# Kernel tuning notes

Measured on AMD Instinct MI355X. Metric: run time of the kernel, lower is better.

Reference implementation:

```python
import jax, jax.numpy as jnp
import numpy as np

N = 50000      # nodes per graph
E = 800000     # edges per graph (avg degree 16)
IN = 128       # in_dim
OUT = 64       # out_dim
HEADS = 2      # second GCNConv out = OUT*HEADS = 128
FILL = 2.0     # improved=True self-loop weight


def setup_inputs():
    key = jax.random.key(0)
    ks = jax.random.split(key, 10)
    x1 = jax.random.normal(ks[0], (N, IN), jnp.float32)
    edge_index1 = jax.random.randint(ks[1], (2, E), 0, N)
    edge_weight1 = jax.random.uniform(ks[2], (E,), jnp.float32)
    x2 = jax.random.normal(ks[3], (N, IN), jnp.float32)
    edge_index2 = jax.random.randint(ks[4], (2, E), 0, N)
    edge_weight2 = jax.random.uniform(ks[5], (E,), jnp.float32)
    # shared tower params (source bug: gcn1 used for both inputs)
    W1 = jax.random.normal(ks[6], (IN, OUT), jnp.float32) / np.sqrt(IN)
    b1 = jnp.zeros((OUT,), jnp.float32)
    W2 = jax.random.normal(ks[7], (OUT, OUT * HEADS), jnp.float32) / np.sqrt(OUT)
    b2 = jnp.zeros((OUT * HEADS,), jnp.float32)
    return {"x1": x1, "edge_index1": edge_index1, "edge_weight1": edge_weight1,
            "x2": x2, "edge_index2": edge_index2, "edge_weight2": edge_weight2,
            "W1": W1, "b1": b1, "W2": W2, "b2": b2}


def _gcn_conv(x, src, dst, ew, W, b, n):
    # GCNConv(improved=True, add_self_loops=True, aggr='max')
    loop = jnp.arange(n)
    src = jnp.concatenate([src, loop])
    dst = jnp.concatenate([dst, loop])
    ew = jnp.concatenate([ew, jnp.full((n,), FILL, ew.dtype)])
    # symmetric gcn normalization
    deg = jax.ops.segment_sum(ew, dst, num_segments=n)
    dinv = jnp.where(deg > 0, jax.lax.rsqrt(jnp.maximum(deg, 1e-30)), 0.0)
    norm = dinv[src] * ew * dinv[dst]          # [E+N]
    h = x @ W                                   # [N, F_out]
    msg = norm[:, None] * h[src]                # [E+N, F_out] gathered messages
    out = jax.ops.segment_max(msg, dst, num_segments=n)  # scatter-max
    out = jnp.where(jnp.isfinite(out), out, 0.0)          # guard empty segments
    return out + b


def _tower(x, ei, ew, W1, b1, W2, b2):
    ew = jax.nn.relu(ew)
    h = _gcn_conv(x, ei[0], ei[1], ew, W1, b1, x.shape[0])
    return _gcn_conv(h, ei[0], ei[1], ew, W2, b2, x.shape[0])


def reference(x1, edge_index1, edge_weight1, x2, edge_index2, edge_weight2, W1, b1, W2, b2):
    g1 = _tower(x1, edge_index1, edge_weight1, W1, b1, W2, b2)
    g2 = _tower(x2, edge_index2, edge_weight2, W1, b1, W2, b2)
    return (g1, g2)
```

## Files before the change

### kernel.cpp

```cpp
#include <hip/hip_runtime.h>
#include <hip/hip_fp16.h>

static constexpr float FILLW = 2.0f;
static constexpr int BSH  = 6;
static constexpr int CAPB = 1792;
static constexpr int NPB  = 256;
static constexpr int EPT  = 8;

__device__ __forceinline__ unsigned pk_mul(unsigned a, unsigned b){
    unsigned r; asm("v_pk_mul_f16 %0, %1, %2" : "=v"(r) : "v"(a), "v"(b)); return r;
}
__device__ __forceinline__ unsigned pk_max(unsigned a, unsigned b){
    unsigned r; asm("v_pk_max_f16 %0, %1, %2" : "=v"(r) : "v"(a), "v"(b)); return r;
}

template<int F, int K, int TR, int KC, bool SCALE, typename OutT>
__device__ __forceinline__ void gemm_tile(const float* __restrict__ A,
        const float* __restrict__ W, OutT* __restrict__ C,
        const float* __restrict__ dv, int rb, int N,
        float* __restrict__ Ws, float* __restrict__ As){
    constexpr int NCH = K / KC;
    constexpr int TRp = TR;
    constexpr int CG  = F / 8;
    constexpr int LPT = TR * KC / 1024;
    const int tid = threadIdx.x;
    for (int i = tid; i < K * F / 4; i += 256)
        ((float4*)Ws)[i] = ((const float4*)W)[i];
    const int tx = tid % CG, ty = tid / CG;
    const int c0 = tx * 8, r0 = ty * 8;

    float acc[8][8];
    #pragma unroll
    for (int i = 0; i < 8; ++i)
        #pragma unroll
        for (int j = 0; j < 8; ++j) acc[i][j] = 0.f;

    float4 st[LPT];
    auto gload = [&](int kc){
        #pragma unroll
        for (int l2 = 0; l2 < LPT; ++l2){
            int l = l2 * 256 + tid;
            int r = l / (KC / 4);
            int kk = (l % (KC / 4)) * 4;
            int ar = rb + r; if (ar >= N) ar = N - 1;
            st[l2] = *(const float4*)(A + (size_t)ar * K + kc * KC + kk);
        }
    };
    auto swrite = [&](int buf){
        float* p = As + buf * (KC * TRp);
        #pragma unroll
        for (int l2 = 0; l2 < LPT; ++l2){
            int l = l2 * 256 + tid;
            int r = l / (KC / 4);
            int kk = (l % (KC / 4)) * 4;
            p[(kk+0)*TRp + r] = st[l2].x;
            p[(kk+1)*TRp + r] = st[l2].y;
            p[(kk+2)*TRp + r] = st[l2].z;
            p[(kk+3)*TRp + r] = st[l2].w;
        }
    };

    gload(0); swrite(0);
    __syncthreads();
    for (int kc = 0; kc < NCH; ++kc){
        if (kc + 1 < NCH) gload(kc + 1);
        const float* Ab = As + (kc & 1) * (KC * TRp);
        #pragma unroll
        for (int j = 0; j < KC; ++j){
            const float* wrow = Ws + (kc * KC + j) * F + c0;
            float4 w0 = *(const float4*)(wrow);
            float4 w1 = *(const float4*)(wrow + 4);
            float4 a0 = *(const float4*)(Ab + j * TRp + r0);
            float4 a1 = *(const float4*)(Ab + j * TRp + r0 + 4);
            float av[8] = {a0.x,a0.y,a0.z,a0.w,a1.x,a1.y,a1.z,a1.w};
            float wvv[8] = {w0.x,w0.y,w0.z,w0.w,w1.x,w1.y,w1.z,w1.w};
            #pragma unroll
            for (int rr = 0; rr < 8; ++rr)
                #pragma unroll
                for (int cc = 0; cc < 8; ++cc)
                    acc[rr][cc] = fmaf(av[rr], wvv[cc], acc[rr][cc]);
        }
        if (kc + 1 < NCH){ swrite((kc + 1) & 1); __syncthreads(); }
    }
    #pragma unroll
    for (int rr = 0; rr < 8; ++rr){
        int row = rb + r0 + rr;
        if (row < N){
            float scv = 1.0f;
            if constexpr (SCALE) scv = dv[row];
            if constexpr (sizeof(OutT) == 2){
                __half2 o2[4];
                #pragma unroll
                for (int q = 0; q < 4; ++q)
                    o2[q] = __floats2half2_rn(acc[rr][2*q]*scv, acc[rr][2*q+1]*scv);
                *(float4*)((__half*)C + (size_t)row * F + c0) = *(float4*)o2;
            } else {
                float4 o0 = {acc[rr][0]*scv, acc[rr][1]*scv, acc[rr][2]*scv, acc[rr][3]*scv};
                float4 o1 = {acc[rr][4]*scv, acc[rr][5]*scv, acc[rr][6]*scv, acc[rr][7]*scv};
                *(float4*)((float*)C + (size_t)row * F + c0)     = o0;
                *(float4*)((float*)C + (size_t)row * F + c0 + 4) = o1;
            }
        }
    }
}

__device__ __forceinline__ void xcd_map(int c, int TW2, int LIN_BPT,
                                        int& t, int& chunk){
    if (TW2){ int x = c & 7; t = x >> 2; chunk = (c >> 3) * 4 + (x & 3); }
    else    { t = c / LIN_BPT; chunk = c - t * LIN_BPT; }
}

__global__ void __launch_bounds__(256) k_cg1(const float* __restrict__ x0,
        const float* __restrict__ x1, const float* __restrict__ W1,
        __half* __restrict__ h0, __half* __restrict__ h1,
        const int* __restrict__ dst0, const int* __restrict__ dst1,
        int* __restrict__ cnts,
        int N, int E, int BPT, int GB, int B1, int TW2){
    __shared__ float Ws[64 * 128];
    __shared__ float As[2 * 8 * 256];
    if ((int)blockIdx.x < GB){
        int t  = (int)blockIdx.x / BPT;
        int rb = ((int)blockIdx.x - t * BPT) * 256;
        gemm_tile<64,128,256,8,false,__half>(t ? x1 : x0, W1, t ? h1 : h0,
                                             nullptr, rb, N, Ws, As);
        return;
    }
    int t, blk;
    xcd_map((int)blockIdx.x - GB, TW2, NPB, t, blk);
    const int* dst = t ? dst1 : dst0;
    int* hist = (int*)Ws;
    const int tid = threadIdx.x;
    for (int i = tid; i < B1; i += 256) hist[i] = 0;
    __syncthreads();
    int per = (E + NPB - 1) / NPB;
    int e0 = blk * per;
    int e1 = e0 + per; if (e1 > E) e1 = E;
    for (int e = e0 + tid; e < e1; e += 256 * EPT){
        int dl[EPT];
        #pragma unroll
        for (int q = 0; q < EPT; ++q){ int ee = e + q*256; dl[q] = (ee < e1) ? dst[ee] : -1; }
        #pragma unroll
        for (int q = 0; q < EPT; ++q) if (dl[q] >= 0) atomicAdd(&hist[dl[q] >> BSH], 1);
    }
    __syncthreads();
    int* co = cnts + (size_t)(t * NPB + blk) * B1;
    for (int i = tid; i < B1; i += 256) co[i] = hist[i];
}

__global__ void __launch_bounds__(64) k_scanR(int* __restrict__ cnts,
        int* __restrict__ gcnt, int B1){
    int bid = (int)blockIdx.x;
    int t = bid / B1, b = bid % B1;
    int lane = threadIdx.x;
    int* cp = cnts + (size_t)t * NPB * B1 + b;
    int x[4];
    #pragma unroll
    for (int j = 0; j < 4; ++j) x[j] = cp[(size_t)(lane * 4 + j) * B1];
    int s = x[0] + x[1] + x[2] + x[3];
    int sc = s;
    #pragma unroll
    for (int o = 1; o < 64; o <<= 1){ int u = __shfl_up(sc, o); if (lane >= o) sc += u; }
    int e0 = sc - s;
    int e1 = e0 + x[0], e2 = e1 + x[1], e3 = e2 + x[2];
    cp[(size_t)(lane * 4 + 0) * B1] = e0;
    cp[(size_t)(lane * 4 + 1) * B1] = e1;
    cp[(size_t)(lane * 4 + 2) * B1] = e2;
    cp[(size_t)(lane * 4 + 3) * B1] = e3;
    if (lane == 63) gcnt[t * B1 + b] = sc;
}

__global__ void __launch_bounds__(256) k_scatter(const int* __restrict__ src0,
        const int* __restrict__ src1,
        const int* __restrict__ dst0, const int* __restrict__ dst1,
        const float* __restrict__ ew0, const float* __restrict__ ew1,
        const int* __restrict__ cnts, uint2* __restrict__ stage,
        int N, int E, int B1, int TW2){
    __shared__ int hist[1024];
    int t, blk;
    xcd_map((int)blockIdx.x, TW2, NPB, t, blk);
    const int* src = t ? src1 : src0;
    const int* dst = t ? dst1 : dst0;
    const float* ew = t ? ew1 : ew0;
    uint2* stg = stage + (size_t)t * B1 * CAPB;
    const int* co = cnts + (size_t)(t * NPB + blk) * B1;
    const int tid = threadIdx.x;
    for (int i = tid; i < B1; i += 256) hist[i] = co[i];
    __syncthreads();
    int per = (E + NPB - 1) / NPB;
    int e0 = blk * per;
    int e1 = e0 + per; if (e1 > E) e1 = E;
    for (int e = e0 + tid; e < e1; e += 256 * EPT){
        int dl[EPT], sl[EPT]; float wl[EPT];
        #pragma unroll
        for (int q = 0; q < EPT; ++q){
            int ee = e + q*256;
            if (ee < e1){ dl[q] = dst[ee]; sl[q] = src[ee]; wl[q] = fmaxf(ew[ee], 0.f); }
            else dl[q] = -1;
        }
        int r[EPT];
        #pragma unroll
        for (int q = 0; q < EPT; ++q)
            if (dl[q] >= 0) r[q] = atomicAdd(&hist[dl[q] >> BSH], 1);
        #pragma unroll
        for (int q = 0; q < EPT; ++q)
            if (dl[q] >= 0 && r[q] < CAPB)
                stg[(size_t)(dl[q] >> BSH) * CAPB + r[q]] =
                    make_uint2(__float_as_uint(wl[q]),
                               (unsigned)sl[q] | ((unsigned)(dl[q] & 63) << 16));
    }
}

__global__ void __launch_bounds__(256) k_pack(const uint2* __restrict__ stage,
        const int* __restrict__ gcnt, int* __restrict__ woff,
        uint2* __restrict__ sn, float* __restrict__ dinv,
        __half* __restrict__ h1, int N, int E, int B1, int TW2){
    int t, b;
    xcd_map((int)blockIdx.x, TW2, B1, t, b);
    if (b >= B1) return;
    const int tid = threadIdx.x;
    const uint2* stg = stage + (size_t)t * B1 * CAPB;
    const int* gc = gcnt + t * B1;
    __shared__ int   wsum[4];
    __shared__ int   nh[64];
    __shared__ float nw[64];
    __shared__ int   offs[64];
    __shared__ float dvs[64];
    int acc = 0;
    for (int i = tid; i < b; i += 256) acc += gc[i];
    #pragma unroll
    for (int o = 32; o; o >>= 1) acc += __shfl_down(acc, o);
    int lane = tid & 63, wv = tid >> 6;
    if (lane == 0) wsum[wv] = acc;
    if (tid < 64){ nh[tid] = 0; nw[tid] = 0.f; }
    __syncthreads();
    const int base = wsum[0] + wsum[1] + wsum[2] + wsum[3];
    int cnt = gc[b]; if (cnt > CAPB) cnt = CAPB;

    int   rr[7]; uint2 rec[7];
    #pragma unroll
    for (int q = 0; q < 7; ++q){
        int j = q * 256 + tid;
        if (j < cnt){
            uint2 v = stg[(size_t)b * CAPB + j];
            int nl = (v.y >> 16) & 63;
            rr[q] = atomicAdd(&nh[nl], 1);
            atomicAdd(&nw[nl], __uint_as_float(v.x));
            rec[q] = v;
        } else rec[q].y = 0xFFFFFFFFu;
    }
    __syncthreads();
    if (tid < 64){
        int v = nh[tid], sc = v;
        #pragma unroll
        for (int o = 1; o < 64; o <<= 1){ int u = __shfl_up(sc, o); if (tid >= o) sc += u; }
        offs[tid] = sc - v;
        int n = (b << BSH) + tid;
        float dv = 0.f;
        if (n < N){
            dv = rsqrtf(FILLW + nw[tid]);
            woff[t * N + n] = base + sc - v;
            dinv[t * N + n] = dv;
        }
        dvs[tid] = dv;
    }
    __syncthreads();
    uint2* sno = sn + (size_t)t * E;
    #pragma unroll
    for (int q = 0; q < 7; ++q){
        if (rec[q].y != 0xFFFFFFFFu){
            int nl   = (int)((rec[q].y >> 16) & 63);
            unsigned srcv = rec[q].y & 0xFFFFu;
            __half hw = __float2half(__uint_as_float(rec[q].x));
            unsigned hu = (unsigned)__half_as_ushort(hw);
            sno[(size_t)base + offs[nl] + rr[q]] =
                make_uint2(srcv, hu | (hu << 16));
        }
    }
    __half2* hb = (__half2*)(h1 + ((size_t)t * N + ((size_t)b << BSH)) * 64);
    #pragma unroll
    for (int j = 0; j < 8; ++j){
        int idx = j * 256 + tid;
        int r = idx >> 5, cc = idx & 31;
        if ((b << BSH) + r < N){
            float2 f = __half22float2(hb[r * 32 + cc]);
            float dv = dvs[r];
            hb[r * 32 + cc] = __floats2half2_rn(f.x * dv, f.y * dv);
        }
    }
}

__global__ void __launch_bounds__(256) k_gemm2(const float* __restrict__ A0,
        const float* __restrict__ A1, const float* __restrict__ W,
        __half* __restrict__ C0, __half* __restrict__ C1,
        const float* __restrict__ dinv, int N, int BPT){
    __shared__ float Ws[64 * 128];
    __shared__ float As[2 * 8 * 128];
    int t  = (int)blockIdx.x / BPT;
    int rb = ((int)blockIdx.x - t * BPT) * 128;
    gemm_tile<128,64,128,8,true,__half>(t ? A1 : A0, W, t ? C1 : C0,
                                        dinv + t * N, rb, N, Ws, As);
}

template<int F, int UG>
__global__ void __launch_bounds__(256) k_agg(const int* __restrict__ woff,
        const uint2* __restrict__ sn, const float* __restrict__ dinv,
        const __half* __restrict__ H0, const __half* __restrict__ H1,
        const float* __restrict__ bias, float* __restrict__ O0, float* __restrict__ O1,
        int N, int E, int BPT, int TW2){
    constexpr int LPR = F / 8;
    constexpr int EG  = 64 / LPR;
    const int lane = threadIdx.x & 63, wv = threadIdx.x >> 6;
    int t, chunk;
    xcd_map((int)blockIdx.x, TW2, BPT, t, chunk);
    int n = chunk * 4 + wv;
    if (n >= N) return;
    int g = t * N + n;
    int beg = woff[g];
    int end = (n == N - 1) ? E : woff[g + 1];
    float di = dinv[g];
    int cnt = end - beg;
    const uint2* st = sn + (size_t)t * E;
    const __half* H = t ? H1 : H0;
    float* O = t ? O1 : O0;
    const int fl = lane % LPR;
    const int eg = lane / LPR;

    unsigned acc[4];
    {
        float4 hv = *(const float4*)(H + (size_t)n * F + fl * 8);
        const unsigned* hp = (const unsigned*)&hv;
        const unsigned two2 = 0x40004000u;
        #pragma unroll
        for (int k = 0; k < 4; ++k) acc[k] = pk_mul(hp[k], two2);
    }
    for (int base = 0; base < cnt; base += 64){
        int m = cnt - base; if (m > 64) m = 64;
        uint2 er = make_uint2(0u, 0u);
        if (lane < m) er = st[beg + base + lane];
        int es = (int)er.x;
        int ep = (int)er.y;
        for (int j = 0; j < m; j += EG * UG){
            int sl[UG], wl[UG]; float4 hv[UG];
            #pragma unroll
            for (int u = 0; u < UG; ++u){
                int jj = j + u * EG + eg; if (jj > m - 1) jj = m - 1;
                sl[u] = __shfl(es, jj);
                wl[u] = __shfl(ep, jj);
            }
            #pragma unroll
            for (int u = 0; u < UG; ++u)
                hv[u] = *(const float4*)(H + (size_t)sl[u] * F + fl * 8);
            #pragma unroll
            for (int u = 0; u < UG; ++u){
                const unsigned* hp = (const unsigned*)&hv[u];
                unsigned w2 = (unsigned)wl[u];
                #pragma unroll
                for (int k = 0; k < 4; ++k)
                    acc[k] = pk_max(acc[k], pk_mul(hp[k], w2));
            }
        }
    }
    #pragma unroll
    for (int msk = LPR; msk < 64; msk <<= 1)
        #pragma unroll
        for (int k = 0; k < 4; ++k){
            unsigned o = (unsigned)__shfl_xor((int)acc[k], msk);
            acc[k] = pk_max(acc[k], o);
        }
    if constexpr (F == 128){
        int f0 = fl * 8 + eg * 2;
        float2 f = __half22float2(*(__half2*)&acc[eg]);
        float2 bb = *(const float2*)(bias + f0);
        *(float2*)(O + (size_t)n * F + f0) =
            make_float2(di * f.x + bb.x, di * f.y + bb.y);
    } else {
        int f0 = fl * 8 + eg;
        unsigned av = acc[eg >> 1];
        unsigned short hs = (unsigned short)((eg & 1) ? (av >> 16) : (av & 0xFFFFu));
        float v = __half2float(__ushort_as_half(hs));
        O[(size_t)n * F + f0] = di * v + bias[f0];
    }
}


extern "C" void kernel_launch(void* const* d_in, const int* in_sizes, int n_in,
                              void* d_out, int out_size, void* d_ws, size_t ws_size,
                              hipStream_t stream){
    const int E  = in_sizes[2];
    const int F1 = in_sizes[7];
    const int F2 = in_sizes[9];
    const int IN = in_sizes[6] / F1;
    const int N  = in_sizes[0] / IN;
    const int B1 = (N + 63) >> BSH;

    const float* W1 = (const float*)d_in[6];
    const float* b1 = (const float*)d_in[7];
    const float* W2 = (const float*)d_in[8];
    const float* b2 = (const float*)d_in[9];

    auto need = [&](int G){
        return (size_t)G * E * 8
             + (size_t)G * N * F2 * 2
             + (size_t)G * N * F1 * 4
             + (size_t)G * N * 8
             + (size_t)G * B1 * 4
             + (size_t)G * NPB * B1 * 4
             + 4096;
    };
    const int G = (ws_size >= need(2)) ? 2 : 1;
    const int TW2 = (G == 2);

    uint2*  sn    = (uint2*)d_ws;
    __half* hbuf  = (__half*)(sn + (size_t)G * E);
    float*  out1  = (float*)(hbuf + (size_t)G * N * F2);
    uint2*  stage = (uint2*)out1;
    float*  dinv  = out1 + (size_t)G * N * F1;
    int*    woff  = (int*)(dinv + (size_t)G * N);
    int*    gcnt  = woff + (size_t)G * N;
    int*    cnts  = gcnt + (size_t)G * B1;

    const int BPT1 = (N + 255) / 256;
    const int BPT2 = (N + 127) / 128;
    const int ABT  = (N + 3) / 4;
    const int GB   = G * BPT1;
    const int partGrid = TW2 ? (NPB / 4) * 8          : G * NPB;
    const int packGrid = TW2 ? ((B1 + 3) / 4) * 8     : G * B1;
    const int aggGrid  = TW2 ? ((ABT + 3) / 4) * 8    : G * ABT;

    for (int it = 0; it < 2; it += G){
        int t0 = it, t1 = (G == 2) ? it + 1 : it;
        const float* x0 = (const float*)d_in[t0*3], * x1 = (const float*)d_in[t1*3];
        const int* ei0 = (const int*)d_in[t0*3+1], * ei1 = (const int*)d_in[t1*3+1];
        const float* ew0 = (const float*)d_in[t0*3+2], * ew1 = (const float*)d_in[t1*3+2];
        const int* src0 = ei0, * dst0 = ei0 + E;
        const int* src1 = ei1, * dst1 = ei1 + E;
        __half* h1_0 = hbuf, * h1_1 = hbuf + (size_t)(G-1) * N * F1;
        __half* h2_0 = hbuf, * h2_1 = hbuf + (size_t)(G-1) * N * F2;
        float* o1_0 = out1, * o1_1 = out1 + (size_t)(G-1) * N * F1;
        float* go0 = (float*)d_out + (size_t)t0 * N * F2;
        float* go1 = (float*)d_out + (size_t)t1 * N * F2;

        k_cg1<<<GB + partGrid, 256, 0, stream>>>(x0, x1, W1, h1_0, h1_1,
                                                 dst0, dst1, cnts, N, E, BPT1, GB, B1, TW2);
        k_scanR<<<G * B1, 64, 0, stream>>>(cnts, gcnt, B1);
        k_scatter<<<partGrid, 256, 0, stream>>>(src0, src1, dst0, dst1, ew0, ew1,
                                                cnts, stage, N, E, B1, TW2);
        k_pack<<<packGrid, 256, 0, stream>>>(stage, gcnt, woff, sn, dinv, hbuf,
                                             N, E, B1, TW2);
        k_agg<64,4><<<aggGrid, 256, 0, stream>>>(woff, sn, dinv, h1_0, h1_1, b1,
                                                 o1_0, o1_1, N, E, ABT, TW2);
        k_gemm2<<<G * BPT2, 256, 0, stream>>>(o1_0, o1_1, W2, h2_0, h2_1, dinv, N, BPT2);
        k_agg<128,4><<<aggGrid, 256, 0, stream>>>(woff, sn, dinv, h2_0, h2_1, b2,
                                                  go0, go1, N, E, ABT, TW2);
    }
}
```

Baseline: 318.5 us.

## Fuse histogram, scan and scatter via global atomic bucket offsets

Replaces the per-block count write, the separate scan kernel and the separate scatter kernel with in-kernel reservation of bucket ranges through atomicAdd on global bucket counters. This is followed directly by scattering edges into staging within the same kernel. It removes two kernel launches and the per-block count matrix traffic, at the cost of global atomic contention (mitigated by rotating bucket order per block) and nondeterministic edge order within buckets. A memset zeroes the counters each iteration. The first aggregation's second template parameter is also reduced from 4 to 2.

```diff
diff --git a/kernel.cpp b/kernel.cpp
--- a/kernel.cpp
+++ b/kernel.cpp
@@ -113,8 +113,10 @@
 __global__ void __launch_bounds__(256) k_cg1(const float* __restrict__ x0,
         const float* __restrict__ x1, const float* __restrict__ W1,
         __half* __restrict__ h0, __half* __restrict__ h1,
+        const int* __restrict__ src0, const int* __restrict__ src1,
         const int* __restrict__ dst0, const int* __restrict__ dst1,
-        int* __restrict__ cnts,
+        const float* __restrict__ ew0, const float* __restrict__ ew1,
+        uint2* __restrict__ stage, int* __restrict__ gcnt,
         int N, int E, int BPT, int GB, int B1, int TW2){
     __shared__ float Ws[64 * 128];
     __shared__ float As[2 * 8 * 256];
@@ -127,7 +129,11 @@
     }
     int t, blk;
     xcd_map((int)blockIdx.x - GB, TW2, NPB, t, blk);
+    const int* src = t ? src1 : src0;
     const int* dst = t ? dst1 : dst0;
+    const float* ew = t ? ew1 : ew0;
+    uint2* stg = stage + (size_t)t * B1 * CAPB;
+    int* gc = gcnt + t * B1;
     int* hist = (int*)Ws;
     const int tid = threadIdx.x;
     for (int i = tid; i < B1; i += 256) hist[i] = 0;
@@ -143,52 +149,13 @@
         for (int q = 0; q < EPT; ++q) if (dl[q] >= 0) atomicAdd(&hist[dl[q] >> BSH], 1);
     }
     __syncthreads();
-    int* co = cnts + (size_t)(t * NPB + blk) * B1;
-    for (int i = tid; i < B1; i += 256) co[i] = hist[i];
-}
-
-__global__ void __launch_bounds__(64) k_scanR(int* __restrict__ cnts,
-        int* __restrict__ gcnt, int B1){
-    int bid = (int)blockIdx.x;
-    int t = bid / B1, b = bid % B1;
-    int lane = threadIdx.x;
-    int* cp = cnts + (size_t)t * NPB * B1 + b;
-    int x[4];
-    #pragma unroll
-    for (int j = 0; j < 4; ++j) x[j] = cp[(size_t)(lane * 4 + j) * B1];
-    int s = x[0] + x[1] + x[2] + x[3];
-    int sc = s;
-    #pragma unroll
-    for (int o = 1; o < 64; o <<= 1){ int u = __shfl_up(sc, o); if (lane >= o) sc += u; }
-    int e0 = sc - s;
-    int e1 = e0 + x[0], e2 = e1 + x[1], e3 = e2 + x[2];
-    cp[(size_t)(lane * 4 + 0) * B1] = e0;
-    cp[(size_t)(lane * 4 + 1) * B1] = e1;
-    cp[(size_t)(lane * 4 + 2) * B1] = e2;
-    cp[(size_t)(lane * 4 + 3) * B1] = e3;
-    if (lane == 63) gcnt[t * B1 + b] = sc;
-}
-
-__global__ void __launch_bounds__(256) k_scatter(const int* __restrict__ src0,
-        const int* __restrict__ src1,
-        const int* __restrict__ dst0, const int* __restrict__ dst1,
-        const float* __restrict__ ew0, const float* __restrict__ ew1,
-        const int* __restrict__ cnts, uint2* __restrict__ stage,
-        int N, int E, int B1, int TW2){
-    __shared__ int hist[1024];
-    int t, blk;
-    xcd_map((int)blockIdx.x, TW2, NPB, t, blk);
-    const int* src = t ? src1 : src0;
-    const int* dst = t ? dst1 : dst0;
-    const float* ew = t ? ew1 : ew0;
-    uint2* stg = stage + (size_t)t * B1 * CAPB;
-    const int* co = cnts + (size_t)(t * NPB + blk) * B1;
-    const int tid = threadIdx.x;
-    for (int i = tid; i < B1; i += 256) hist[i] = co[i];
-    __syncthreads();
-    int per = (E + NPB - 1) / NPB;
-    int e0 = blk * per;
-    int e1 = e0 + per; if (e1 > E) e1 = E;
+    int rot = (blk * 193) % B1;
+    for (int i = tid; i < B1; i += 256){
+        int b = i + rot; if (b >= B1) b -= B1;
+        int h = hist[b];
+        hist[b] = h ? atomicAdd(&gc[b], h) : 0;
+    }
+    __syncthreads();
     for (int e = e0 + tid; e < e1; e += 256 * EPT){
         int dl[EPT], sl[EPT]; float wl[EPT];
         #pragma unroll
@@ -404,7 +371,6 @@
              + (size_t)G * N * F1 * 4
              + (size_t)G * N * 8
              + (size_t)G * B1 * 4
-             + (size_t)G * NPB * B1 * 4
              + 4096;
     };
     const int G = (ws_size >= need(2)) ? 2 : 1;
@@ -417,7 +383,6 @@
     float*  dinv  = out1 + (size_t)G * N * F1;
     int*    woff  = (int*)(dinv + (size_t)G * N);
     int*    gcnt  = woff + (size_t)G * N;
-    int*    cnts  = gcnt + (size_t)G * B1;
 
     const int BPT1 = (N + 255) / 256;
     const int BPT2 = (N + 127) / 128;
@@ -440,14 +405,13 @@
         float* go0 = (float*)d_out + (size_t)t0 * N * F2;
         float* go1 = (float*)d_out + (size_t)t1 * N * F2;
 
+        hipMemsetAsync(gcnt, 0, (size_t)G * B1 * sizeof(int), stream);
         k_cg1<<<GB + partGrid, 256, 0, stream>>>(x0, x1, W1, h1_0, h1_1,
-                                                 dst0, dst1, cnts, N, E, BPT1, GB, B1, TW2);
-        k_scanR<<<G * B1, 64, 0, stream>>>(cnts, gcnt, B1);
-        k_scatter<<<partGrid, 256, 0, stream>>>(src0, src1, dst0, dst1, ew0, ew1,
-                                                cnts, stage, N, E, B1, TW2);
+                                                 src0, src1, dst0, dst1, ew0, ew1,
+                                                 stage, gcnt, N, E, BPT1, GB, B1, TW2);
         k_pack<<<packGrid, 256, 0, stream>>>(stage, gcnt, woff, sn, dinv, hbuf,
                                              N, E, B1, TW2);
-        k_agg<64,4><<<aggGrid, 256, 0, stream>>>(woff, sn, dinv, h1_0, h1_1, b1,
+        k_agg<64,2><<<aggGrid, 256, 0, stream>>>(woff, sn, dinv, h1_0, h1_1, b1,
                                                  o1_0, o1_1, N, E, ABT, TW2);
         k_gemm2<<<G * BPT2, 256, 0, stream>>>(o1_0, o1_1, W2, h2_0, h2_1, dinv, N, BPT2);
         k_agg<128,4><<<aggGrid, 256, 0, stream>>>(woff, sn, dinv, h2_0, h2_1, b2,
```

Result: faster. 301.5 us, median of 2 (-5.3%).
